# Kernel optimization log

Hardware: AMD Instinct MI355X
Metric: run time of the kernel (lower is better)

## Reference

```python
import jax, jax.numpy as jnp
import numpy as np

EPS = 1e-5
OUTPUT_BINS = 1000


def _act_quant(x):
    # per-token absmax int8 quantization (BitNet b1.58)
    scale = 127.0 / jnp.clip(jnp.max(jnp.abs(x), axis=-1, keepdims=True), EPS, None)
    return jnp.clip(jnp.round(x * scale), -128.0, 127.0) / scale


def _weight_quant(w):
    # ternary absmean quantization
    scale = 1.0 / jnp.clip(jnp.mean(jnp.abs(w)), EPS, None)
    return jnp.clip(jnp.round(w * scale), -1.0, 1.0) / scale


def _ste(x, q):
    return x + jax.lax.stop_gradient(q - x)


def bitlinear(x, w):
    xq = _ste(x, _act_quant(x))
    wq = _ste(w, _weight_quant(w))
    return jnp.einsum('bi,oi->bo', xq, wq)


def layernorm(x, g, b):
    mu = jnp.mean(x, axis=-1, keepdims=True)
    var = jnp.mean(jnp.square(x - mu), axis=-1, keepdims=True)
    return (x - mu) * jax.lax.rsqrt(var + EPS) * g + b


def setup_inputs() -> dict:
    key = jax.random.key(0)
    ks = jax.random.split(key, 5)
    B, D_IN, H = 4096, 1024, 4096
    return {
        'x': jax.random.normal(ks[0], (B, D_IN), dtype=jnp.float32),
        'W0': jax.random.normal(ks[1], (H, D_IN), dtype=jnp.float32) * 0.02,
        'W1': jax.random.normal(ks[2], (H, H), dtype=jnp.float32) * 0.02,
        'W2': jax.random.normal(ks[3], (H, H), dtype=jnp.float32) * 0.02,
        'W3': jax.random.normal(ks[4], (2 * OUTPUT_BINS, H), dtype=jnp.float32) * 0.02,
        'g0': jnp.ones((H,), jnp.float32), 'b0': jnp.zeros((H,), jnp.float32),
        'g1': jnp.ones((H,), jnp.float32), 'b1': jnp.zeros((H,), jnp.float32),
        'g2': jnp.ones((H,), jnp.float32), 'b2': jnp.zeros((H,), jnp.float32),
    }


def reference(x, W0, W1, W2, W3, g0, b0, g1, b1, g2, b2):
    h = jax.nn.silu(layernorm(bitlinear(x, W0), g0, b0))
    h = jax.nn.silu(layernorm(bitlinear(h, W1), g1, b1))
    h = jax.nn.silu(layernorm(bitlinear(h, W2), g2, b2))
    out = bitlinear(h, W3)                      # [B, 2*output_bins]
    mz_logits, int_logits = jnp.split(out, 2, axis=-1)
    mz_values = jax.nn.sigmoid(mz_logits) * (OUTPUT_BINS - 1) + 1.0
    intensities = jax.nn.sigmoid(int_logits) * 100.0
    return (mz_values, intensities)
```

## Files before the change

kernel.cpp:

```cpp
#include <hip/hip_runtime.h>
#include <hip/hip_bf16.h>
#include <cstdint>
#include <cstddef>

#define EPS 1e-5f

typedef __attribute__((ext_vector_type(4))) int int32x4;
typedef __attribute__((ext_vector_type(16))) int int32x16;

__device__ __forceinline__ float blk_sum(float v, float* s4) {
    #pragma unroll
    for (int o = 32; o; o >>= 1) v += __shfl_down(v, o, 64);
    if ((threadIdx.x & 63) == 0) s4[threadIdx.x >> 6] = v;
    __syncthreads();
    v = s4[0] + s4[1] + s4[2] + s4[3];
    __syncthreads();
    return v;
}

__device__ __forceinline__ void blk_sum2(float& a, float& b, float* s8) {
    #pragma unroll
    for (int o = 32; o; o >>= 1) {
        a += __shfl_down(a, o, 64);
        b += __shfl_down(b, o, 64);
    }
    if ((threadIdx.x & 63) == 0) {
        s8[threadIdx.x >> 6] = a;
        s8[4 + (threadIdx.x >> 6)] = b;
    }
    __syncthreads();
    a = s8[0] + s8[1] + s8[2] + s8[3];
    b = s8[4] + s8[5] + s8[6] + s8[7];
    __syncthreads();
}

__device__ __forceinline__ float blk_max(float v, float* s4) {
    #pragma unroll
    for (int o = 32; o; o >>= 1) v = fmaxf(v, __shfl_down(v, o, 64));
    if ((threadIdx.x & 63) == 0) s4[threadIdx.x >> 6] = v;
    __syncthreads();
    v = fmaxf(fmaxf(s4[0], s4[1]), fmaxf(s4[2], s4[3]));
    __syncthreads();
    return v;
}

__device__ __forceinline__ int pack4(float a, float b, float c, float d, float lo, float hi) {
    int x0 = (int)fminf(fmaxf(a, lo), hi);
    int x1 = (int)fminf(fmaxf(b, lo), hi);
    int x2 = (int)fminf(fmaxf(c, lo), hi);
    int x3 = (int)fminf(fmaxf(d, lo), hi);
    return (x0 & 255) | ((x1 & 255) << 8) | ((x2 & 255) << 16) | ((x3 & 255) << 24);
}

__device__ __forceinline__ float bflo(unsigned u) { return __uint_as_float(u << 16); }
__device__ __forceinline__ float bfhi(unsigned u) { return __uint_as_float(u & 0xffff0000u); }

__global__ __launch_bounds__(256) void absmean_all_kernel(
    const float* __restrict__ W0, const float* __restrict__ W1,
    const float* __restrict__ W2, const float* __restrict__ W3,
    float* __restrict__ sums) {
    __shared__ float s4[4];
    const float* w; long long n4; int sidx, nb, lb;
    int bx = blockIdx.x;
    if (bx < 1024)      { w = W0; n4 = 1048576;  sidx = 0; nb = 1024; lb = bx; }
    else if (bx < 3072) { w = W1; n4 = 4194304;  sidx = 1; nb = 2048; lb = bx - 1024; }
    else if (bx < 5120) { w = W2; n4 = 4194304;  sidx = 2; nb = 2048; lb = bx - 3072; }
    else                { w = W3; n4 = 2048000;  sidx = 3; nb = 1024; lb = bx - 5120; }
    const float4* w4 = (const float4*)w;
    float s = 0.f;
    for (long long i = (long long)lb * 256 + threadIdx.x; i < n4; i += (long long)nb * 256) {
        float4 v = w4[i];
        s += fabsf(v.x) + fabsf(v.y) + fabsf(v.z) + fabsf(v.w);
    }
    s = blk_sum(s, s4);
    if (threadIdx.x == 0) atomicAdd(&sums[sidx], s);
}

__global__ __launch_bounds__(256) void wquant_all_kernel(
    const float* __restrict__ W0, const float* __restrict__ W1,
    const float* __restrict__ W2, const float* __restrict__ W3,
    int* __restrict__ q0, int* __restrict__ q1, int* __restrict__ q2, int* __restrict__ q3,
    const float* __restrict__ sums) {
    const float* w; int* q; long long n4, pn4; int sidx, nb, lb; float invN;
    int bx = blockIdx.x;
    if (bx < 1024)      { w = W0; q = q0; n4 = 1048576;  pn4 = 1048576; sidx = 0; nb = 1024; lb = bx;        invN = 1.f / 4194304.f; }
    else if (bx < 3072) { w = W1; q = q1; n4 = 4194304;  pn4 = 4194304; sidx = 1; nb = 2048; lb = bx - 1024; invN = 1.f / 16777216.f; }
    else if (bx < 5120) { w = W2; q = q2; n4 = 4194304;  pn4 = 4194304; sidx = 2; nb = 2048; lb = bx - 3072; invN = 1.f / 16777216.f; }
    else                { w = W3; q = q3; n4 = 2048000;  pn4 = 2097152; sidx = 3; nb = 1024; lb = bx - 5120; invN = 1.f / 8192000.f; }
    float mean = fmaxf(sums[sidx] * invN, EPS);
    float scale = 1.f / mean;
    const float4* w4 = (const float4*)w;
    for (long long i = (long long)lb * 256 + threadIdx.x; i < pn4; i += (long long)nb * 256) {
        if (i < n4) {
            float4 v = w4[i];
            q[i] = pack4(rintf(v.x * scale), rintf(v.y * scale),
                         rintf(v.z * scale), rintf(v.w * scale), -1.f, 1.f);
        } else {
            q[i] = 0;
        }
    }
}

__global__ __launch_bounds__(256) void actquant_kernel(const float* __restrict__ x,
                                                       int* __restrict__ q,
                                                       float* __restrict__ inv_s) {
    __shared__ float s4[4];
    int row = blockIdx.x;
    const float4* xr = (const float4*)(x + (size_t)row * 1024);
    float4 v = xr[threadIdx.x];
    float m = fmaxf(fmaxf(fabsf(v.x), fabsf(v.y)), fmaxf(fabsf(v.z), fabsf(v.w)));
    m = blk_max(m, s4);
    m = fmaxf(m, EPS);
    float scale = 127.f / m;
    if (threadIdx.x == 0) inv_s[row] = m / 127.f;
    q[(size_t)row * 256 + threadIdx.x] =
        pack4(rintf(v.x * scale), rintf(v.y * scale),
              rintf(v.z * scale), rintf(v.w * scale), -128.f, 127.f);
}

__global__ __launch_bounds__(256) void ln_silu_quant_kernel(const ushort* __restrict__ h,
                                                            const float* __restrict__ g,
                                                            const float* __restrict__ b,
                                                            int* __restrict__ q,
                                                            float* __restrict__ inv_s) {
    __shared__ float s8[8];
    int row = blockIdx.x;
    int t = threadIdx.x;
    const uint4* hr = (const uint4*)(h + (size_t)row * 4096);
    uint4 p0 = hr[t * 2], p1 = hr[t * 2 + 1];
    float f[16];
    f[0] = bflo(p0.x); f[1] = bfhi(p0.x); f[2] = bflo(p0.y); f[3] = bfhi(p0.y);
    f[4] = bflo(p0.z); f[5] = bfhi(p0.z); f[6] = bflo(p0.w); f[7] = bfhi(p0.w);
    f[8] = bflo(p1.x); f[9] = bfhi(p1.x); f[10] = bflo(p1.y); f[11] = bfhi(p1.y);
    f[12] = bflo(p1.z); f[13] = bfhi(p1.z); f[14] = bflo(p1.w); f[15] = bfhi(p1.w);
    float sum = 0.f, sq = 0.f;
    #pragma unroll
    for (int i = 0; i < 16; i++) { sum += f[i]; sq += f[i] * f[i]; }
    blk_sum2(sum, sq, s8);
    float mu = sum * (1.f / 4096.f);
    float var = sq * (1.f / 4096.f) - mu * mu;
    float rs = rsqrtf(var + EPS);
    const float4* g4 = (const float4*)g;
    const float4* b4 = (const float4*)b;
    float amax = 0.f;
    #pragma unroll
    for (int i = 0; i < 4; i++) {
        float4 gg = g4[t * 4 + i];
        float4 bb = b4[t * 4 + i];
        float y0 = (f[i * 4 + 0] - mu) * rs * gg.x + bb.x;
        float y1 = (f[i * 4 + 1] - mu) * rs * gg.y + bb.y;
        float y2 = (f[i * 4 + 2] - mu) * rs * gg.z + bb.z;
        float y3 = (f[i * 4 + 3] - mu) * rs * gg.w + bb.w;
        f[i * 4 + 0] = y0 / (1.f + expf(-y0));
        f[i * 4 + 1] = y1 / (1.f + expf(-y1));
        f[i * 4 + 2] = y2 / (1.f + expf(-y2));
        f[i * 4 + 3] = y3 / (1.f + expf(-y3));
    }
    #pragma unroll
    for (int i = 0; i < 16; i++) amax = fmaxf(amax, fabsf(f[i]));
    amax = blk_max(amax, s8);
    amax = fmaxf(amax, EPS);
    float scale = 127.f / amax;
    if (t == 0) inv_s[row] = amax / 127.f;
    int4 o;
    o.x = pack4(rintf(f[0] * scale), rintf(f[1] * scale), rintf(f[2] * scale), rintf(f[3] * scale), -128.f, 127.f);
    o.y = pack4(rintf(f[4] * scale), rintf(f[5] * scale), rintf(f[6] * scale), rintf(f[7] * scale), -128.f, 127.f);
    o.z = pack4(rintf(f[8] * scale), rintf(f[9] * scale), rintf(f[10] * scale), rintf(f[11] * scale), -128.f, 127.f);
    o.w = pack4(rintf(f[12] * scale), rintf(f[13] * scale), rintf(f[14] * scale), rintf(f[15] * scale), -128.f, 127.f);
    ((int4*)((char*)q + (size_t)row * 4096))[t] = o;
}

__device__ __forceinline__ void load_lds16(const void* g, void* l) {
    __builtin_amdgcn_global_load_lds((__attribute__((address_space(1))) void*)(g),
                                     (__attribute__((address_space(3))) void*)(l), 16, 0, 0);
}

template <int MODE>
__global__ __launch_bounds__(256, 4) void gemm_i8_kernel(
    const char* __restrict__ A, const char* __restrict__ B,
    const float* __restrict__ inv_s, const float* __restrict__ wsum, float invWN,
    int K, void* __restrict__ outp) {
    __shared__ __align__(16) char lA[128 * 64];
    __shared__ __align__(16) char lB[128 * 64];
    const int t = threadIdx.x;
    const int lane = t & 63;
    const int wave = t >> 6;
    const int bm = blockIdx.y * 128, bn = blockIdx.x * 128;
    const int wr = (wave >> 1) * 64, wc = (wave & 1) * 64;

    int32x16 acc[2][2] = {};

    const int r0 = t >> 2;
    const int c0 = (t & 3) * 16;
    const char* gA0 = A + (size_t)(bm + r0) * K + c0;
    const char* gA1 = A + (size_t)(bm + r0 + 64) * K + c0;
    const char* gB0 = B + (size_t)(bn + r0) * K + c0;
    const char* gB1 = B + (size_t)(bn + r0 + 64) * K + c0;
    char* sA0 = lA + t * 16;
    char* sA1 = lA + 4096 + t * 16;
    char* sB0 = lB + t * 16;
    char* sB1 = lB + 4096 + t * 16;

    const int r = lane & 31;
    const int q = lane >> 5;
    const char* pA0 = lA + (wr + r) * 64 + q * 16;
    const char* pA1 = pA0 + 32 * 64;
    const char* pB0 = lB + (wc + r) * 64 + q * 16;
    const char* pB1 = pB0 + 32 * 64;

    for (int k0 = 0; k0 < K; k0 += 64) {
        load_lds16(gA0 + k0, sA0);
        load_lds16(gA1 + k0, sA1);
        load_lds16(gB0 + k0, sB0);
        load_lds16(gB1 + k0, sB1);
        __syncthreads();

        #pragma unroll
        for (int ks = 0; ks < 2; ks++) {
            int32x4 a0 = *(const int32x4*)(pA0 + ks * 32);
            int32x4 a1 = *(const int32x4*)(pA1 + ks * 32);
            int32x4 b0 = *(const int32x4*)(pB0 + ks * 32);
            int32x4 b1 = *(const int32x4*)(pB1 + ks * 32);
            acc[0][0] = __builtin_amdgcn_mfma_i32_32x32x32_i8(a0, b0, acc[0][0], 0, 0, 0);
            acc[0][1] = __builtin_amdgcn_mfma_i32_32x32x32_i8(a0, b1, acc[0][1], 0, 0, 0);
            acc[1][0] = __builtin_amdgcn_mfma_i32_32x32x32_i8(a1, b0, acc[1][0], 0, 0, 0);
            acc[1][1] = __builtin_amdgcn_mfma_i32_32x32x32_i8(a1, b1, acc[1][1], 0, 0, 0);
        }
        __syncthreads();
    }

    const float wmean = fmaxf(wsum[0] * invWN, EPS);
    #pragma unroll
    for (int mt = 0; mt < 2; mt++) {
        #pragma unroll
        for (int reg = 0; reg < 16; reg++) {
            int gr = bm + wr + mt * 32 + 4 * q + (reg & 3) + 8 * (reg >> 2);
            float rowscale = inv_s[gr] * wmean;
            #pragma unroll
            for (int nt = 0; nt < 2; nt++) {
                int gc = bn + wc + nt * 32 + r;
                float v = (float)acc[mt][nt][reg] * rowscale;
                if (MODE == 0) {
                    ((__hip_bfloat16*)outp)[(size_t)gr * 4096 + gc] = __float2bfloat16(v);
                } else {
                    if (gc < 2000) {
                        float sg = 1.f / (1.f + expf(-v));
                        float* out = (float*)outp;
                        if (gc < 1000)
                            out[(size_t)gr * 1000 + gc] = sg * 999.f + 1.f;
                        else
                            out[(size_t)4096 * 1000 + (size_t)gr * 1000 + (gc - 1000)] =
                                sg * 100.f;
                    }
                }
            }
        }
    }
}

extern "C" void kernel_launch(void* const* d_in, const int* in_sizes, int n_in,
                              void* d_out, int out_size, void* d_ws, size_t ws_size,
                              hipStream_t stream) {
    const float* x  = (const float*)d_in[0];
    const float* W0 = (const float*)d_in[1];
    const float* W1 = (const float*)d_in[2];
    const float* W2 = (const float*)d_in[3];
    const float* W3 = (const float*)d_in[4];
    const float* g0 = (const float*)d_in[5];
    const float* b0 = (const float*)d_in[6];
    const float* g1 = (const float*)d_in[7];
    const float* b1 = (const float*)d_in[8];
    const float* g2 = (const float*)d_in[9];
    const float* b2 = (const float*)d_in[10];
    float* out = (float*)d_out;

    char* ws = (char*)d_ws;
    size_t off = 0;
    auto alloc = [&](size_t bytes) -> char* {
        char* p = ws + off;
        off = (off + bytes + 255) & ~(size_t)255;
        return p;
    };
    float* sums = (float*)alloc(4 * sizeof(float));
    float* inv0 = (float*)alloc(4096 * 4);
    float* inv1 = (float*)alloc(4096 * 4);
    float* inv2 = (float*)alloc(4096 * 4);
    float* inv3 = (float*)alloc(4096 * 4);
    char* wq0 = alloc(4096ll * 1024);
    char* wq1 = alloc(4096ll * 4096);
    char* wq2 = alloc(4096ll * 4096);
    char* wq3 = alloc(2048ll * 4096);
    char* a0  = alloc(4096ll * 1024);
    char* a1  = alloc(4096ll * 4096);
    char* a2  = alloc(4096ll * 4096);
    char* h   = alloc(4096ll * 4096 * 2);
    char* a3 = a1;

    hipMemsetAsync(sums, 0, 4 * sizeof(float), stream);

    absmean_all_kernel<<<6144, 256, 0, stream>>>(W0, W1, W2, W3, sums);
    actquant_kernel<<<4096, 256, 0, stream>>>(x, (int*)a0, inv0);
    wquant_all_kernel<<<6144, 256, 0, stream>>>(W0, W1, W2, W3, (int*)wq0, (int*)wq1,
                                                (int*)wq2, (int*)wq3, sums);

    gemm_i8_kernel<0><<<dim3(32, 32), 256, 0, stream>>>(a0, wq0, inv0, sums + 0,
                                                        1.f / 4194304.f, 1024, h);
    ln_silu_quant_kernel<<<4096, 256, 0, stream>>>((const ushort*)h, g0, b0, (int*)a1, inv1);

    gemm_i8_kernel<0><<<dim3(32, 32), 256, 0, stream>>>(a1, wq1, inv1, sums + 1,
                                                        1.f / 16777216.f, 4096, h);
    ln_silu_quant_kernel<<<4096, 256, 0, stream>>>((const ushort*)h, g1, b1, (int*)a2, inv2);

    gemm_i8_kernel<0><<<dim3(32, 32), 256, 0, stream>>>(a2, wq2, inv2, sums + 2,
                                                        1.f / 16777216.f, 4096, h);
    ln_silu_quant_kernel<<<4096, 256, 0, stream>>>((const ushort*)h, g2, b2, (int*)a3, inv3);

    gemm_i8_kernel<1><<<dim3(16, 32), 256, 0, stream>>>(a3, wq3, inv3, sums + 3,
                                                        1.f / 8192000.f, 4096, out);
}
```

Measured before the change: 612.4 us.

## Switch int8 GEMM to 16x16x64 MFMA with 128-wide K tiles and XOR-swizzled LDS

Replaces the 32x32x32 int8 MFMA tiling with 16x16x64 MFMAs over a 4x4 fragment grid per wave, and doubles the K step per LDS stage to 128. Global-to-LDS loads use an XOR column swizzle so the fragment reads avoid LDS bank conflicts. The aim is fewer syncs per K, higher MFMA density and conflict-free LDS reads. The cost is twice the LDS per block and a lower launch-bounds occupancy hint of 2.

```diff
diff --git a/kernel.cpp b/kernel.cpp
--- a/kernel.cpp
+++ b/kernel.cpp
@@ -6,7 +6,6 @@
 #define EPS 1e-5f
 
 typedef __attribute__((ext_vector_type(4))) int int32x4;
-typedef __attribute__((ext_vector_type(16))) int int32x16;
 
 __device__ __forceinline__ float blk_sum(float v, float* s4) {
     #pragma unroll
@@ -176,70 +175,74 @@
 }
 
 template <int MODE>
-__global__ __launch_bounds__(256, 4) void gemm_i8_kernel(
+__global__ __launch_bounds__(256, 2) void gemm_i8_kernel(
     const char* __restrict__ A, const char* __restrict__ B,
     const float* __restrict__ inv_s, const float* __restrict__ wsum, float invWN,
     int K, void* __restrict__ outp) {
-    __shared__ __align__(16) char lA[128 * 64];
-    __shared__ __align__(16) char lB[128 * 64];
+    __shared__ __align__(16) char lA[128 * 128];
+    __shared__ __align__(16) char lB[128 * 128];
     const int t = threadIdx.x;
     const int lane = t & 63;
     const int wave = t >> 6;
     const int bm = blockIdx.y * 128, bn = blockIdx.x * 128;
     const int wr = (wave >> 1) * 64, wc = (wave & 1) * 64;
 
-    int32x16 acc[2][2] = {};
-
-    const int r0 = t >> 2;
-    const int c0 = (t & 3) * 16;
-    const char* gA0 = A + (size_t)(bm + r0) * K + c0;
-    const char* gA1 = A + (size_t)(bm + r0 + 64) * K + c0;
-    const char* gB0 = B + (size_t)(bn + r0) * K + c0;
-    const char* gB1 = B + (size_t)(bn + r0 + 64) * K + c0;
-    char* sA0 = lA + t * 16;
-    char* sA1 = lA + 4096 + t * 16;
-    char* sB0 = lB + t * 16;
-    char* sB1 = lB + 4096 + t * 16;
-
-    const int r = lane & 31;
-    const int q = lane >> 5;
-    const char* pA0 = lA + (wr + r) * 64 + q * 16;
-    const char* pA1 = pA0 + 32 * 64;
-    const char* pB0 = lB + (wc + r) * 64 + q * 16;
-    const char* pB1 = pB0 + 32 * 64;
-
-    for (int k0 = 0; k0 < K; k0 += 64) {
-        load_lds16(gA0 + k0, sA0);
-        load_lds16(gA1 + k0, sA1);
-        load_lds16(gB0 + k0, sB0);
-        load_lds16(gB1 + k0, sB1);
+    int32x4 acc[4][4] = {};
+
+    const int r0 = t >> 3;
+    const int c0 = (t & 7) * 16;
+    const int gcol = c0 ^ (16 * (r0 & 7));
+    const char* gA = A + (size_t)(bm + r0) * K + gcol;
+    const char* gB = B + (size_t)(bn + r0) * K + gcol;
+    char* sA = lA + t * 16;
+    char* sB = lB + t * 16;
+
+    const int fr = lane & 15;
+    const int fq = lane >> 4;
+    const int swz = 16 * (fr & 7);
+
+    for (int k0 = 0; k0 < K; k0 += 128) {
+        #pragma unroll
+        for (int j = 0; j < 4; j++)
+            load_lds16(gA + (size_t)(j * 32) * K + k0, sA + j * 4096);
+        #pragma unroll
+        for (int j = 0; j < 4; j++)
+            load_lds16(gB + (size_t)(j * 32) * K + k0, sB + j * 4096);
         __syncthreads();
 
         #pragma unroll
         for (int ks = 0; ks < 2; ks++) {
-            int32x4 a0 = *(const int32x4*)(pA0 + ks * 32);
-            int32x4 a1 = *(const int32x4*)(pA1 + ks * 32);
-            int32x4 b0 = *(const int32x4*)(pB0 + ks * 32);
-            int32x4 b1 = *(const int32x4*)(pB1 + ks * 32);
-            acc[0][0] = __builtin_amdgcn_mfma_i32_32x32x32_i8(a0, b0, acc[0][0], 0, 0, 0);
-            acc[0][1] = __builtin_amdgcn_mfma_i32_32x32x32_i8(a0, b1, acc[0][1], 0, 0, 0);
-            acc[1][0] = __builtin_amdgcn_mfma_i32_32x32x32_i8(a1, b0, acc[1][0], 0, 0, 0);
-            acc[1][1] = __builtin_amdgcn_mfma_i32_32x32x32_i8(a1, b1, acc[1][1], 0, 0, 0);
+            const int col = (ks * 64 + fq * 16) ^ swz;
+            int32x4 af[4], bf[4];
+            #pragma unroll
+            for (int mt = 0; mt < 4; mt++)
+                af[mt] = *(const int32x4*)(lA + (wr + mt * 16 + fr) * 128 + col);
+            #pragma unroll
+            for (int nt = 0; nt < 4; nt++)
+                bf[nt] = *(const int32x4*)(lB + (wc + nt * 16 + fr) * 128 + col);
+            #pragma unroll
+            for (int mt = 0; mt < 4; mt++) {
+                #pragma unroll
+                for (int nt = 0; nt < 4; nt++) {
+                    acc[mt][nt] = __builtin_amdgcn_mfma_i32_16x16x64_i8(af[mt], bf[nt],
+                                                                        acc[mt][nt], 0, 0, 0);
+                }
+            }
         }
         __syncthreads();
     }
 
     const float wmean = fmaxf(wsum[0] * invWN, EPS);
     #pragma unroll
-    for (int mt = 0; mt < 2; mt++) {
+    for (int mt = 0; mt < 4; mt++) {
         #pragma unroll
-        for (int reg = 0; reg < 16; reg++) {
-            int gr = bm + wr + mt * 32 + 4 * q + (reg & 3) + 8 * (reg >> 2);
+        for (int rg = 0; rg < 4; rg++) {
+            int gr = bm + wr + mt * 16 + fq * 4 + rg;
             float rowscale = inv_s[gr] * wmean;
             #pragma unroll
-            for (int nt = 0; nt < 2; nt++) {
-                int gc = bn + wc + nt * 32 + r;
-                float v = (float)acc[mt][nt][reg] * rowscale;
+            for (int nt = 0; nt < 4; nt++) {
+                int gc = bn + wc + nt * 16 + fr;
+                float v = (float)acc[mt][nt][rg] * rowscale;
                 if (MODE == 0) {
                     ((__hip_bfloat16*)outp)[(size_t)gr * 4096 + gc] = __float2bfloat16(v);
                 } else {
```

Measured after the change: 545.2 us. -11.0%, faster.
